# Kernel optimization log

Hardware: AMD Instinct MI355X
Metric: run time of the kernel (lower is better)

Reference implementation:

```python
import jax, jax.numpy as jnp
import numpy as np

N, M, DIM_K, DIM_V = 8192, 8192, 256, 256

def setup_inputs() -> dict:
    key = jax.random.key(0)
    kq, kk, kv = jax.random.split(key, 3)
    Q = jax.random.normal(kq, (N, DIM_K), dtype=jnp.float32)
    K = jax.random.normal(kk, (M, DIM_K), dtype=jnp.float32)
    V = jax.random.normal(kv, (M, DIM_V), dtype=jnp.float32)
    return {"Q": Q, "K": K, "V": V}

def reference(Q, K, V):
    # scores: [N, M] = Q @ K^T / sqrt(dim_k)
    scale = 1.0 / jnp.sqrt(jnp.asarray(Q.shape[-1], dtype=Q.dtype))
    scores = jnp.einsum('nd,md->nm', Q, K) * scale
    attn = jax.nn.softmax(scores, axis=-1)  # softmax over keys
    return attn @ V  # [N, dim_v]
```

## Files before the change

### kernel.cpp

```cpp
#include <hip/hip_runtime.h>
#include <hip/hip_bf16.h>
#include <hip/hip_fp16.h>


typedef __attribute__((ext_vector_type(16))) float floatx16;
typedef __attribute__((ext_vector_type(8)))  short short8;

union S8u { short8 v; unsigned short u[8]; };

#if __has_builtin(__builtin_amdgcn_exp2f)
#define EXP2F(x) __builtin_amdgcn_exp2f(x)
#else
#define EXP2F(x) exp2f(x)
#endif

__device__ __forceinline__ unsigned short f2bf(float f) {
    unsigned int u = __builtin_bit_cast(unsigned int, f);
    unsigned int r = u + 0x7fffu + ((u >> 16) & 1u);
    return (unsigned short)(r >> 16);
}

__device__ __forceinline__ unsigned cvtpk_bf16(float lo, float hi) {
    unsigned r;
    asm("v_cvt_pk_bf16_f32 %0, %1, %2" : "=v"(r) : "v"(lo), "v"(hi));
    return r;
}

__device__ __forceinline__ void gload16(const void* g, void* l) {
    __builtin_amdgcn_global_load_lds(
        (const __attribute__((address_space(1))) unsigned int*)g,
        (__attribute__((address_space(3))) unsigned int*)l, 16, 0, 0);
}


__global__ void cvt_bf16_kernel(const float* __restrict__ in,
                                unsigned short* __restrict__ out,
                                float scale, int n8) {
    int i = blockIdx.x * blockDim.x + threadIdx.x;
    if (i >= n8) return;
    const float4* p = reinterpret_cast<const float4*>(in) + (size_t)i * 2;
    float4 a = p[0], b = p[1];
    S8u r;
    r.u[0] = f2bf(a.x * scale); r.u[1] = f2bf(a.y * scale);
    r.u[2] = f2bf(a.z * scale); r.u[3] = f2bf(a.w * scale);
    r.u[4] = f2bf(b.x * scale); r.u[5] = f2bf(b.y * scale);
    r.u[6] = f2bf(b.z * scale); r.u[7] = f2bf(b.w * scale);
    *reinterpret_cast<short8*>(out + (size_t)i * 8) = r.v;
}

__global__ void transpose_v_kernel(const float* __restrict__ V,
                                   unsigned short* __restrict__ Vt) {
    __shared__ unsigned short T[64][72];
    const int kv0 = blockIdx.x * 64;
    const int v0  = blockIdx.y * 64;
    const int tid = threadIdx.x;
#pragma unroll
    for (int it = 0; it < 4; ++it) {
        int flat = it * 256 + tid;
        int r  = flat >> 4;
        int c4 = (flat & 15) * 4;
        float4 f = *reinterpret_cast<const float4*>(
            V + (size_t)(kv0 + r) * 256 + v0 + c4);
        T[c4 + 0][r] = f2bf(f.x);
        T[c4 + 1][r] = f2bf(f.y);
        T[c4 + 2][r] = f2bf(f.z);
        T[c4 + 3][r] = f2bf(f.w);
    }
    __syncthreads();
#pragma unroll
    for (int it = 0; it < 2; ++it) {
        int flat = it * 256 + tid;
        int r  = flat >> 3;
        int c8 = (flat & 7) * 8;
        short8 v8 = *reinterpret_cast<const short8*>(&T[r][c8]);
        *reinterpret_cast<short8*>(Vt + (size_t)(v0 + r) * 8192 + kv0 + c8) = v8;
    }
}


__global__ __launch_bounds__(512, 2)
void attn_kernel(const float* __restrict__ Qf,
                 const unsigned short* __restrict__ Kb,
                 const unsigned short* __restrict__ VtG,
                 __half* __restrict__ Opart,
                 float* __restrict__ Ml,
                 int kv_span, int gshift) {
    __shared__ __align__(16) unsigned char lds[2][65536];

    const int tid  = threadIdx.x;
    const int lane = tid & 63;
    const int w    = tid >> 6;
    const int l31  = lane & 31;
    const int h    = lane >> 5;

    const int ngm1 = (1 << gshift) - 1;
    const int id   = blockIdx.x + 32 * blockIdx.y;
    const int g    = id & ngm1;
    const int qblk = id >> gshift;
    const int kv_begin = g * kv_span;
    const int tiles = kv_span >> 6;
    const int q0 = qblk * 256 + w * 32;

    const float qs = 0.09016844005556021f;
    short8 qf[16];
    {
        const float* qp = Qf + (size_t)(q0 + l31) * 256 + h * 8;
#pragma unroll
        for (int ds = 0; ds < 16; ++ds) {
            float4 f0 = *reinterpret_cast<const float4*>(qp + ds * 16);
            float4 f1 = *reinterpret_cast<const float4*>(qp + ds * 16 + 4);
            uint4 uu;
            uu.x = cvtpk_bf16(f0.x * qs, f0.y * qs);
            uu.y = cvtpk_bf16(f0.z * qs, f0.w * qs);
            uu.z = cvtpk_bf16(f1.x * qs, f1.y * qs);
            uu.w = cvtpk_bf16(f1.z * qs, f1.w * qs);
            qf[ds] = __builtin_bit_cast(short8, uu);
        }
    }

    floatx16 o[8];
#pragma unroll
    for (int vt = 0; vt < 8; ++vt)
#pragma unroll
        for (int r = 0; r < 16; ++r) o[vt][r] = 0.f;
    float m_run = -1e30f, l_run = 0.f;

    int offk[4], offv[4];
#pragma unroll
    for (int i = 0; i < 4; ++i) {
        int j  = w * 4 + i;
        int rk = j * 2 + (lane >> 5);
        int ck = (lane & 31) ^ (rk & 7);
        offk[i] = rk * 256 + ck * 8;
        int rv = j * 8 + (lane >> 3);
        int cv = (lane & 7) ^ (rv & 7);
        offv[i] = rv * 8192 + cv * 8;
    }

    auto STAGE = [&](int kv0, int bufsel) {
        unsigned char* kb = &lds[bufsel][0];
        unsigned char* vb = &lds[bufsel][32768];
        const unsigned short* ks = Kb + (size_t)kv0 * 256;
        const unsigned short* vs = VtG + kv0;
#pragma unroll
        for (int i = 0; i < 4; ++i) {
            int j = w * 4 + i;
            gload16(ks + offk[i], kb + j * 1024);
            gload16(vs + offv[i], vb + j * 1024);
        }
    };

    STAGE(kv_begin, 0);
    asm volatile("s_waitcnt vmcnt(0)" ::: "memory");
    __syncthreads();

    const int swz = l31 & 7;

    for (int t = 0; t < tiles; ++t) {
        const int cur = t & 1;
        if (t + 1 < tiles) STAGE(kv_begin + (t + 1) * 64, cur ^ 1);

        const unsigned char* kl = &lds[cur][0];
        const unsigned char* vl = &lds[cur][32768];

        floatx16 s0, s1;
#pragma unroll
        for (int r = 0; r < 16; ++r) { s0[r] = 0.f; s1[r] = 0.f; }
        __builtin_amdgcn_s_setprio(1);
#pragma unroll
        for (int ds = 0; ds < 16; ++ds) {
            int c0 = (ds * 2 + h) ^ swz;
            short8 a0 = *reinterpret_cast<const short8*>(kl + (size_t)l31 * 512 + c0 * 16);
            short8 a1 = *reinterpret_cast<const short8*>(kl + (size_t)(l31 + 32) * 512 + c0 * 16);
            s0 = __builtin_amdgcn_mfma_f32_32x32x16_bf16(a0, qf[ds], s0, 0, 0, 0);
            s1 = __builtin_amdgcn_mfma_f32_32x32x16_bf16(a1, qf[ds], s1, 0, 0, 0);
        }
        __builtin_amdgcn_s_setprio(0);

        float t8[8];
#pragma unroll
        for (int i = 0; i < 8; ++i)
            t8[i] = fmaxf(fmaxf(s0[i], s0[i + 8]), fmaxf(s1[i], s1[i + 8]));
        float a0m = fmaxf(t8[0], t8[1]), a1m = fmaxf(t8[2], t8[3]);
        float a2m = fmaxf(t8[4], t8[5]), a3m = fmaxf(t8[6], t8[7]);
        float mt = fmaxf(fmaxf(a0m, a1m), fmaxf(a2m, a3m));
        mt = fmaxf(mt, __shfl_xor(mt, 32));
        if (__any(mt > m_run + 11.5f)) {
            float mnew = fmaxf(m_run, mt);
            float al = EXP2F(m_run - mnew);
            m_run = mnew;
            l_run *= al;
#pragma unroll
            for (int reg = 0; reg < 16; ++reg) {
                int srcl = ((reg & 3) + 8 * (reg >> 2)) + 4 * h;
                float alr = __shfl(al, srcl);
#pragma unroll
                for (int vt = 0; vt < 8; ++vt) o[vt][reg] *= alr;
            }
        }
#pragma unroll
        for (int r = 0; r < 16; ++r) s0[r] = EXP2F(s0[r] - m_run);
#pragma unroll
        for (int r = 0; r < 16; ++r) s1[r] = EXP2F(s1[r] - m_run);
        float u[8];
#pragma unroll
        for (int i = 0; i < 8; ++i)
            u[i] = (s0[i] + s0[i + 8]) + (s1[i] + s1[i + 8]);
        float lt = ((u[0] + u[1]) + (u[2] + u[3])) + ((u[4] + u[5]) + (u[6] + u[7]));
        lt += __shfl_xor(lt, 32);
        l_run += lt;

        auto buildPA = [&](const floatx16& sv, int rbase) -> short8 {
            unsigned cpk0 = cvtpk_bf16(sv[rbase + 0], sv[rbase + 1]);
            unsigned cpk1 = cvtpk_bf16(sv[rbase + 2], sv[rbase + 3]);
            unsigned cpk2 = cvtpk_bf16(sv[rbase + 4], sv[rbase + 5]);
            unsigned cpk3 = cvtpk_bf16(sv[rbase + 6], sv[rbase + 7]);
            uint4 uu;
#if __has_builtin(__builtin_amdgcn_permlane32_swap)
            auto r02 = __builtin_amdgcn_permlane32_swap((int)cpk0, (int)cpk2, false, false);
            auto r13 = __builtin_amdgcn_permlane32_swap((int)cpk1, (int)cpk3, false, false);
            uu.x = (unsigned)r02[0]; uu.y = (unsigned)r13[0];
            uu.z = (unsigned)r02[1]; uu.w = (unsigned)r13[1];
#else
            unsigned send0 = h ? cpk0 : cpk2;
            unsigned send1 = h ? cpk1 : cpk3;
            unsigned r0 = (unsigned)__shfl_xor((int)send0, 32);
            unsigned r1 = (unsigned)__shfl_xor((int)send1, 32);
            uu.x = h ? r0 : cpk0;
            uu.y = h ? r1 : cpk1;
            uu.z = h ? cpk2 : r0;
            uu.w = h ? cpk3 : r1;
#endif
            return __builtin_bit_cast(short8, uu);
        };

        __builtin_amdgcn_s_setprio(1);
#pragma unroll
        for (int kk = 0; kk < 4; ++kk) {
            short8 pa = buildPA((kk < 2) ? s0 : s1, (kk & 1) * 8);
            int cv = (kk * 2 + h) ^ swz;
#pragma unroll
            for (int vt = 0; vt < 8; ++vt) {
                short8 b = *reinterpret_cast<const short8*>(
                    vl + (size_t)(vt * 32 + l31) * 128 + cv * 16);
                o[vt] = __builtin_amdgcn_mfma_f32_32x32x16_bf16(pa, b, o[vt], 0, 0, 0);
            }
        }
        __builtin_amdgcn_s_setprio(0);

        asm volatile("s_waitcnt vmcnt(0)" ::: "memory");
        __syncthreads();
    }

    const size_t gq = (size_t)g * 8192;
    float linv = 1.0f / l_run;
#pragma unroll
    for (int reg = 0; reg < 16; ++reg) {
        int row = (reg & 3) + 8 * (reg >> 2) + 4 * h;
        float li = __shfl(linv, row);
#pragma unroll
        for (int vt = 0; vt < 8; ++vt)
            Opart[(gq + q0 + row) * 256 + vt * 32 + l31] =
                __float2half_rn(o[vt][reg] * li);
    }
    if (h == 0) {
        size_t idx = (gq + q0 + l31) * 2;
        Ml[idx]     = m_run;
        Ml[idx + 1] = l_run;
    }
}


__global__ void merge_kernel(const __half* __restrict__ Opart,
                             const float* __restrict__ Ml,
                             float* __restrict__ out, int ngroups) {
    int row = blockIdx.x;
    int col = threadIdx.x;
    float m = -1e30f;
    for (int g = 0; g < ngroups; ++g)
        m = fmaxf(m, Ml[((size_t)g * 8192 + row) * 2]);
    float den = 0.f, acc = 0.f;
    for (int g = 0; g < ngroups; ++g) {
        float wg = EXP2F(Ml[((size_t)g * 8192 + row) * 2] - m) *
                   Ml[((size_t)g * 8192 + row) * 2 + 1];
        den += wg;
        acc += wg * __half2float(Opart[((size_t)g * 8192 + row) * 256 + col]);
    }
    out[(size_t)row * 256 + col] = acc / den;
}


extern "C" void kernel_launch(void* const* d_in, const int* in_sizes, int n_in,
                              void* d_out, int out_size, void* d_ws, size_t ws_size,
                              hipStream_t stream) {
    const float* Q = (const float*)d_in[0];
    const float* K = (const float*)d_in[1];
    const float* V = (const float*)d_in[2];
    float* out = (float*)d_out;

    unsigned short* Kb = (unsigned short*)d_ws;
    unsigned short* Vt = Kb + (size_t)8192 * 256;

    const size_t base = (size_t)8192 * 256 * 2 * 2;
    const size_t osz  = (size_t)8192 * 256 * 2;
    const size_t mlsz = (size_t)8192 * 2 * 4;

    int gshift = 3;
    for (; gshift > 0; --gshift)
        if (base + ((osz + mlsz) << gshift) <= ws_size) break;
    int ng = 1 << gshift;

    __half* Opart = (__half*)((char*)d_ws + base);
    float*  Mlp   = (float*)((char*)d_ws + base + osz * (size_t)ng);

    const int n8 = 8192 * 256 / 8;
    cvt_bf16_kernel<<<n8 / 256, 256, 0, stream>>>(K, Kb, 1.0f, n8);
    transpose_v_kernel<<<dim3(128, 4), 256, 0, stream>>>(V, Vt);
    attn_kernel<<<dim3(32, ng), 512, 0, stream>>>(Q, Kb, Vt, Opart, Mlp,
                                                  8192 / ng, gshift);
    merge_kernel<<<8192, 256, 0, stream>>>(Opart, Mlp, out, ng);
}
```

Before: 137.1 us.

## Split KV tile softmax into two halves to interleave QK, softmax and PV MFMAs

Each 64-key tile is now processed as two 32-key halves. Online-softmax max/exp/sum runs per half, and the second half's QK^T MFMAs are issued before the first half's PV MFMAs. The goal is to overlap exp and VALU softmax work with matrix-core work within a wave and to shorten the dependency chain. The trade-off is more frequent rescale checks and max reductions per tile, and possibly more register pressure from keeping s1 live alongside the PV accumulation.

```diff
diff --git a/kernel.cpp b/kernel.cpp
--- a/kernel.cpp
+++ b/kernel.cpp
@@ -78,6 +78,8 @@
 }
 
 
+#define MFMA_B16 __builtin_amdgcn_mfma_f32_32x32x16_bf16
+
 __global__ __launch_bounds__(512, 2)
 void attn_kernel(const float* __restrict__ Qf,
                  const unsigned short* __restrict__ Kb,
@@ -156,34 +158,37 @@
 
     const int swz = l31 & 7;
 
-    for (int t = 0; t < tiles; ++t) {
-        const int cur = t & 1;
-        if (t + 1 < tiles) STAGE(kv_begin + (t + 1) * 64, cur ^ 1);
-
-        const unsigned char* kl = &lds[cur][0];
-        const unsigned char* vl = &lds[cur][32768];
-
-        floatx16 s0, s1;
-#pragma unroll
-        for (int r = 0; r < 16; ++r) { s0[r] = 0.f; s1[r] = 0.f; }
-        __builtin_amdgcn_s_setprio(1);
-#pragma unroll
-        for (int ds = 0; ds < 16; ++ds) {
-            int c0 = (ds * 2 + h) ^ swz;
-            short8 a0 = *reinterpret_cast<const short8*>(kl + (size_t)l31 * 512 + c0 * 16);
-            short8 a1 = *reinterpret_cast<const short8*>(kl + (size_t)(l31 + 32) * 512 + c0 * 16);
-            s0 = __builtin_amdgcn_mfma_f32_32x32x16_bf16(a0, qf[ds], s0, 0, 0, 0);
-            s1 = __builtin_amdgcn_mfma_f32_32x32x16_bf16(a1, qf[ds], s1, 0, 0, 0);
-        }
-        __builtin_amdgcn_s_setprio(0);
-
-        float t8[8];
-#pragma unroll
-        for (int i = 0; i < 8; ++i)
-            t8[i] = fmaxf(fmaxf(s0[i], s0[i + 8]), fmaxf(s1[i], s1[i + 8]));
-        float a0m = fmaxf(t8[0], t8[1]), a1m = fmaxf(t8[2], t8[3]);
-        float a2m = fmaxf(t8[4], t8[5]), a3m = fmaxf(t8[6], t8[7]);
-        float mt = fmaxf(fmaxf(a0m, a1m), fmaxf(a2m, a3m));
+    auto buildPA = [&](const floatx16& sv, int rbase) -> short8 {
+        unsigned cpk0 = cvtpk_bf16(sv[rbase + 0], sv[rbase + 1]);
+        unsigned cpk1 = cvtpk_bf16(sv[rbase + 2], sv[rbase + 3]);
+        unsigned cpk2 = cvtpk_bf16(sv[rbase + 4], sv[rbase + 5]);
+        unsigned cpk3 = cvtpk_bf16(sv[rbase + 6], sv[rbase + 7]);
+        uint4 uu;
+#if __has_builtin(__builtin_amdgcn_permlane32_swap)
+        auto r02 = __builtin_amdgcn_permlane32_swap((int)cpk0, (int)cpk2, false, false);
+        auto r13 = __builtin_amdgcn_permlane32_swap((int)cpk1, (int)cpk3, false, false);
+        uu.x = (unsigned)r02[0]; uu.y = (unsigned)r13[0];
+        uu.z = (unsigned)r02[1]; uu.w = (unsigned)r13[1];
+#else
+        unsigned send0 = h ? cpk0 : cpk2;
+        unsigned send1 = h ? cpk1 : cpk3;
+        unsigned r0 = (unsigned)__shfl_xor((int)send0, 32);
+        unsigned r1 = (unsigned)__shfl_xor((int)send1, 32);
+        uu.x = h ? r0 : cpk0;
+        uu.y = h ? r1 : cpk1;
+        uu.z = h ? cpk2 : r0;
+        uu.w = h ? cpk3 : r1;
+#endif
+        return __builtin_bit_cast(short8, uu);
+    };
+
+    auto SM_HALF = [&](floatx16& sv) {
+        float t4[4];
+#pragma unroll
+        for (int i = 0; i < 4; ++i)
+            t4[i] = fmaxf(fmaxf(sv[i], sv[i + 4]),
+                          fmaxf(sv[i + 8], sv[i + 12]));
+        float mt = fmaxf(fmaxf(t4[0], t4[1]), fmaxf(t4[2], t4[3]));
         mt = fmaxf(mt, __shfl_xor(mt, 32));
         if (__any(mt > m_run + 11.5f)) {
             float mnew = fmaxf(m_run, mt);
@@ -199,51 +204,77 @@
             }
         }
 #pragma unroll
-        for (int r = 0; r < 16; ++r) s0[r] = EXP2F(s0[r] - m_run);
-#pragma unroll
-        for (int r = 0; r < 16; ++r) s1[r] = EXP2F(s1[r] - m_run);
-        float u[8];
-#pragma unroll
-        for (int i = 0; i < 8; ++i)
-            u[i] = (s0[i] + s0[i + 8]) + (s1[i] + s1[i + 8]);
-        float lt = ((u[0] + u[1]) + (u[2] + u[3])) + ((u[4] + u[5]) + (u[6] + u[7]));
+        for (int r = 0; r < 16; ++r) sv[r] = EXP2F(sv[r] - m_run);
+        float u[4];
+#pragma unroll
+        for (int i = 0; i < 4; ++i)
+            u[i] = (sv[i] + sv[i + 4]) + (sv[i + 8] + sv[i + 12]);
+        float lt = (u[0] + u[1]) + (u[2] + u[3]);
         lt += __shfl_xor(lt, 32);
         l_run += lt;
-
-        auto buildPA = [&](const floatx16& sv, int rbase) -> short8 {
-            unsigned cpk0 = cvtpk_bf16(sv[rbase + 0], sv[rbase + 1]);
-            unsigned cpk1 = cvtpk_bf16(sv[rbase + 2], sv[rbase + 3]);
-            unsigned cpk2 = cvtpk_bf16(sv[rbase + 4], sv[rbase + 5]);
-            unsigned cpk3 = cvtpk_bf16(sv[rbase + 6], sv[rbase + 7]);
-            uint4 uu;
-#if __has_builtin(__builtin_amdgcn_permlane32_swap)
-            auto r02 = __builtin_amdgcn_permlane32_swap((int)cpk0, (int)cpk2, false, false);
-            auto r13 = __builtin_amdgcn_permlane32_swap((int)cpk1, (int)cpk3, false, false);
-            uu.x = (unsigned)r02[0]; uu.y = (unsigned)r13[0];
-            uu.z = (unsigned)r02[1]; uu.w = (unsigned)r13[1];
-#else
-            unsigned send0 = h ? cpk0 : cpk2;
-            unsigned send1 = h ? cpk1 : cpk3;
-            unsigned r0 = (unsigned)__shfl_xor((int)send0, 32);
-            unsigned r1 = (unsigned)__shfl_xor((int)send1, 32);
-            uu.x = h ? r0 : cpk0;
-            uu.y = h ? r1 : cpk1;
-            uu.z = h ? cpk2 : r0;
-            uu.w = h ? cpk3 : r1;
-#endif
-            return __builtin_bit_cast(short8, uu);
-        };
-
+    };
+
+    for (int t = 0; t < tiles; ++t) {
+        const int cur = t & 1;
+        if (t + 1 < tiles) STAGE(kv_begin + (t + 1) * 64, cur ^ 1);
+
+        const unsigned char* kl = &lds[cur][0];
+        const unsigned char* vl = &lds[cur][32768];
+
+        floatx16 s0;
+#pragma unroll
+        for (int r = 0; r < 16; ++r) s0[r] = 0.f;
         __builtin_amdgcn_s_setprio(1);
 #pragma unroll
-        for (int kk = 0; kk < 4; ++kk) {
-            short8 pa = buildPA((kk < 2) ? s0 : s1, (kk & 1) * 8);
+        for (int ds = 0; ds < 16; ++ds) {
+            int c0 = (ds * 2 + h) ^ swz;
+            short8 a0 = *reinterpret_cast<const short8*>(
+                kl + (size_t)l31 * 512 + c0 * 16);
+            s0 = MFMA_B16(a0, qf[ds], s0, 0, 0, 0);
+        }
+        __builtin_amdgcn_s_setprio(0);
+
+        SM_HALF(s0);
+
+        floatx16 s1;
+#pragma unroll
+        for (int r = 0; r < 16; ++r) s1[r] = 0.f;
+        __builtin_amdgcn_s_setprio(1);
+#pragma unroll
+        for (int ds = 0; ds < 16; ++ds) {
+            int c0 = (ds * 2 + h) ^ swz;
+            short8 a1 = *reinterpret_cast<const short8*>(
+                kl + (size_t)(l31 + 32) * 512 + c0 * 16);
+            s1 = MFMA_B16(a1, qf[ds], s1, 0, 0, 0);
+        }
+        __builtin_amdgcn_s_setprio(0);
+
+        __builtin_amdgcn_s_setprio(1);
+#pragma unroll
+        for (int kk = 0; kk < 2; ++kk) {
+            short8 pa = buildPA(s0, kk * 8);
             int cv = (kk * 2 + h) ^ swz;
 #pragma unroll
             for (int vt = 0; vt < 8; ++vt) {
                 short8 b = *reinterpret_cast<const short8*>(
                     vl + (size_t)(vt * 32 + l31) * 128 + cv * 16);
-                o[vt] = __builtin_amdgcn_mfma_f32_32x32x16_bf16(pa, b, o[vt], 0, 0, 0);
+                o[vt] = MFMA_B16(pa, b, o[vt], 0, 0, 0);
+            }
+        }
+        __builtin_amdgcn_s_setprio(0);
+
+        SM_HALF(s1);
+
+        __builtin_amdgcn_s_setprio(1);
+#pragma unroll
+        for (int kk = 0; kk < 2; ++kk) {
+            short8 pa = buildPA(s1, kk * 8);
+            int cv = ((kk + 2) * 2 + h) ^ swz;
+#pragma unroll
+            for (int vt = 0; vt < 8; ++vt) {
+                short8 b = *reinterpret_cast<const short8*>(
+                    vl + (size_t)(vt * 32 + l31) * 128 + cv * 16);
+                o[vt] = MFMA_B16(pa, b, o[vt], 0, 0, 0);
             }
         }
         __builtin_amdgcn_s_setprio(0);
```

After: 142.9 us. 4.2% more time.
